# Kernel optimization log

Measured on AMD Instinct MI355X. Metric: run time of the kernel, lower is better.

## Reference

```python
import jax, jax.numpy as jnp
import numpy as np

N_NODES = 50000
N_EDGES = 800000
N_GRAPHS = 1024
H = 128          # hidden_dim
L = 5            # n_conv_layers
NODE_IN = 4
EDGE_IN = 41
N_TARGETS = 3
EPS = 1e-5


def _ln(x, g, b):
    m = jnp.mean(x, axis=-1, keepdims=True)
    v = jnp.var(x, axis=-1, keepdims=True)
    return (x - m) / jnp.sqrt(v + EPS) * g + b


def setup_inputs() -> dict:
    key = jax.random.key(0)
    ks = jax.random.split(key, 24)
    w = lambda k, shp: (jax.random.normal(k, shp, dtype=jnp.float32) * 0.05)
    inp = {
        "atom_fea": jax.random.normal(ks[0], (N_NODES, NODE_IN), dtype=jnp.float32),
        "nbr_fea": jax.random.normal(ks[1], (N_EDGES, EDGE_IN), dtype=jnp.float32),
        "nbr_idx": jax.random.randint(ks[2], (N_EDGES, 2), 0, N_NODES, dtype=jnp.int32),
        "batch_mapping": jnp.sort(jax.random.randint(ks[3], (N_NODES,), 0, N_GRAPHS, dtype=jnp.int32)),
        # node embedding: Linear(4->H) + LayerNorm + SiLU
        "emb_w": w(ks[4], (NODE_IN, H)), "emb_b": jnp.zeros((H,), jnp.float32),
        "emb_ln_g": jnp.ones((H,), jnp.float32), "emb_ln_b": jnp.zeros((H,), jnp.float32),
        # edge embedding: Linear(41->H) + SiLU
        "edge_w": w(ks[5], (EDGE_IN, H)), "edge_b": jnp.zeros((H,), jnp.float32),
        # conv layers: Linear(2H->2H), SiLU, Linear(2H->H), SiLU; stacked over L
        "conv_w1": w(ks[6], (L, 2 * H, 2 * H)), "conv_b1": jnp.zeros((L, 2 * H), jnp.float32),
        "conv_w2": w(ks[7], (L, 2 * H, H)), "conv_b2": jnp.zeros((L, H), jnp.float32),
        "ln_g": jnp.ones((L, H), jnp.float32), "ln_b": jnp.zeros((L, H), jnp.float32),
        # output head
        "out_w1": w(ks[8], (H, H)), "out_b1": jnp.zeros((H,), jnp.float32),
        "out_w2": w(ks[9], (H, H // 2)), "out_b2": jnp.zeros((H // 2,), jnp.float32),
        "out_w3": w(ks[10], (H // 2, N_TARGETS)), "out_b3": jnp.zeros((N_TARGETS,), jnp.float32),
    }
    return inp


def reference(atom_fea, nbr_fea, nbr_idx, batch_mapping,
              emb_w, emb_b, emb_ln_g, emb_ln_b, edge_w, edge_b,
              conv_w1, conv_b1, conv_w2, conv_b2, ln_g, ln_b,
              out_w1, out_b1, out_w2, out_b2, out_w3, out_b3):
    silu = jax.nn.silu
    # embeddings (dropout is eval-mode identity)
    x = silu(_ln(atom_fea @ emb_w + emb_b, emb_ln_g, emb_ln_b))      # [N, H]
    e = silu(nbr_fea @ edge_w + edge_b)                               # [E, H]
    src, dst = nbr_idx[:, 0], nbr_idx[:, 1]
    n = x.shape[0]
    # per-node incoming edge counts (same every layer)
    cnt = jax.ops.segment_sum(jnp.ones_like(dst, dtype=x.dtype), dst, num_segments=n)
    cnt = jnp.clip(cnt, 1.0)[:, None]
    for i in range(L):
        m = jnp.concatenate([x[src], e], axis=1)                      # [E, 2H] gather
        m = silu(m @ conv_w1[i] + conv_b1[i])                         # [E, 2H]
        m = silu(m @ conv_w2[i] + conv_b2[i])                         # [E, H]
        aggr = jax.ops.segment_sum(m, dst, num_segments=n) / cnt      # scatter-mean
        x = _ln(x + aggr, ln_g[i], ln_b[i])                           # residual + LN
    # graph-level mean pooling
    gcnt = jax.ops.segment_sum(jnp.ones((n,), x.dtype), batch_mapping, num_segments=N_GRAPHS)
    gcnt = jnp.clip(gcnt, 1.0)[:, None]
    crystal = jax.ops.segment_sum(x, batch_mapping, num_segments=N_GRAPHS) / gcnt  # [G, H]
    h = silu(crystal @ out_w1 + out_b1)
    h = silu(h @ out_w2 + out_b2)
    return h @ out_w3 + out_b3                                        # [G, n_targets]
```

## Files before the change

kernel.cpp:

```cpp
#include <hip/hip_runtime.h>
#include <hip/hip_bf16.h>
#include <math.h>

#define N_NODES 50000
#define N_EDGES 800000
#define N_GRAPHS 1024
#define HD 128
#define NLAYERS 5
#define EDGE_IN 41
#define NT 3
#define LN_EPS 1e-5f

typedef unsigned int uint;
typedef unsigned short ushort;
typedef __attribute__((ext_vector_type(8))) short short8;
typedef __attribute__((ext_vector_type(4))) float f32x4;

__device__ __forceinline__ float silu_f(float v) {
    return v * __builtin_amdgcn_rcpf(1.0f + __expf(-v));
}

__device__ __forceinline__ ushort f2bf(float f) {
    uint u = __float_as_uint(f);
    u = u + 0x7FFFu + ((u >> 16) & 1u);
    return (ushort)(u >> 16);
}

__device__ __forceinline__ short8 ld16(const ushort* p) {
    union { int4 i; short8 s; } u;
    u.i = *(const int4*)p;
    return u.s;
}

__device__ __forceinline__ f32x4 mfma16(short8 a, short8 b, f32x4 c) {
    return __builtin_amdgcn_mfma_f32_16x16x32_bf16(a, b, c, 0, 0, 0);
}

__device__ __forceinline__ void wave_lds_fence() {
    __asm__ volatile("s_waitcnt lgkmcnt(0)" ::: "memory");
}

__device__ __forceinline__ void cp16(const ushort* g, ushort* l) {
    __builtin_amdgcn_global_load_lds(
        (const __attribute__((address_space(1))) unsigned int*)g,
        (__attribute__((address_space(3))) unsigned int*)l, 16, 0, 0);
}

__device__ __forceinline__ void stage4k(ushort* lds, const ushort* g, int w, int L) {
#pragma unroll
    for (int i = 0; i < 2; ++i) {
        int f = w * 1024 + i * 512;
        cp16(g + f + L * 8, lds + f);
    }
}

__global__ void k_zero(float* __restrict__ p, int n) {
    int i = blockIdx.x * 256 + threadIdx.x;
    if (i < n) p[i] = 0.0f;
}

__global__ void k_hist(const int* __restrict__ nbr_idx, int* __restrict__ cnt_i) {
    int i = blockIdx.x * 256 + threadIdx.x;
    if (i < N_EDGES) atomicAdd(&cnt_i[nbr_idx[2 * i + 1]], 1);
}

__global__ __launch_bounds__(256) void k_scan(
    const int* __restrict__ cnt_i, int* __restrict__ cur, float* __restrict__ cntf)
{
    __shared__ int warpsum[4];
    __shared__ int srun;
    int tid = threadIdx.x;
    int lane = tid & 63, wv = tid >> 6;
    if (tid == 0) srun = 0;
    __syncthreads();
    for (int base = 0; base < N_NODES; base += 256) {
        int i = base + tid;
        int c = (i < N_NODES) ? cnt_i[i] : 0;
        int s = c;
        for (int off = 1; off < 64; off <<= 1) {
            int t = __shfl_up(s, off);
            if (lane >= off) s += t;
        }
        if (lane == 63) warpsum[wv] = s;
        __syncthreads();
        int woff = 0;
        for (int k = 0; k < wv; ++k) woff += warpsum[k];
        int run = srun;
        if (i < N_NODES) {
            cur[i]  = run + woff + s - c;
            cntf[i] = (float)c;
        }
        __syncthreads();
        if (tid == 255) srun = run + woff + s;
    }
}

__global__ void k_scatter(const int* __restrict__ nbr_idx, int* __restrict__ cur,
                          int* __restrict__ ssrc, int* __restrict__ sdst,
                          int* __restrict__ posof)
{
    int e = blockIdx.x * 256 + threadIdx.x;
    if (e < N_EDGES) {
        int s = nbr_idx[2 * e];
        int d = nbr_idx[2 * e + 1];
        int p = atomicAdd(&cur[d], 1);
        ssrc[p] = s;
        sdst[p] = d;
        posof[e] = p;
    }
}

__global__ void k_swz_w1(const float* __restrict__ w1, ushort* __restrict__ w1s) {
    int i = blockIdx.x * 256 + threadIdx.x;
    int l = i >> 16;
    int r = i & 65535;
    int j = r & 7, L = (r >> 3) & 63, s = (r >> 9) & 7, c = (r >> 12) & 15;
    int k = 32 * s + ((L >> 4) & 3) * 8 + j;
    int n = 16 * c + (L & 15);
    w1s[i] = f2bf(w1[(size_t)l * 65536 + k * 256 + n]);
}
__global__ void k_swz_w2(const float* __restrict__ w2, ushort* __restrict__ w2s) {
    int i = blockIdx.x * 256 + threadIdx.x;
    int l = i >> 15;
    int r = i & 32767;
    int j = r & 7, L = (r >> 3) & 63, t = (r >> 9) & 7, s2 = (r >> 12) & 7;
    int k = 32 * s2 + ((L >> 4) & 3) * 8 + j;
    int n = 16 * t + (L & 15);
    w2s[i] = f2bf(w2[(size_t)l * 32768 + k * 128 + n]);
}

__global__ __launch_bounds__(128) void k_node_embed(
    const float* __restrict__ atom, const float* __restrict__ w,
    const float* __restrict__ b, const float* __restrict__ g,
    const float* __restrict__ bet, float* __restrict__ x, ushort* __restrict__ x_bf)
{
    int node = blockIdx.x;
    int h = threadIdx.x;
    float4 a = *(const float4*)(atom + (size_t)node * 4);
    float acc = b[h] + a.x * w[h] + a.y * w[HD + h] + a.z * w[2 * HD + h] + a.w * w[3 * HD + h];
    __shared__ float s1[2], s2[2];
    float sum = acc, sq = acc * acc;
    for (int off = 32; off > 0; off >>= 1) { sum += __shfl_down(sum, off); sq += __shfl_down(sq, off); }
    int wid = h >> 6, lane = h & 63;
    if (lane == 0) { s1[wid] = sum; s2[wid] = sq; }
    __syncthreads();
    float m = (s1[0] + s1[1]) * (1.0f / 128.0f);
    float v = (s2[0] + s2[1]) * (1.0f / 128.0f) - m * m;
    float y = (acc - m) * rsqrtf(v + LN_EPS) * g[h] + bet[h];
    y = silu_f(y);
    x[(size_t)node * HD + h] = y;
    x_bf[(size_t)node * HD + h] = f2bf(y);
}

#define ETILE 32
__global__ __launch_bounds__(128) void k_edge_embed(
    const float* __restrict__ fea, const float* __restrict__ w,
    const float* __restrict__ b, const int* __restrict__ posof,
    ushort* __restrict__ e_bf)
{
    __shared__ float sf[ETILE][EDGE_IN + 1];
    int e0 = blockIdx.x * ETILE;
    int tid = threadIdx.x;
    for (int i = tid; i < ETILE * EDGE_IN; i += 128) {
        int m = i / EDGE_IN, k = i % EDGE_IN;
        sf[m][k] = fea[(size_t)(e0 + m) * EDGE_IN + k];
    }
    __syncthreads();
    float bb = b[tid];
    float acc[ETILE];
#pragma unroll
    for (int m = 0; m < ETILE; m++) acc[m] = bb;
    for (int k = 0; k < EDGE_IN; k++) {
        float wk = w[k * HD + tid];
#pragma unroll
        for (int m = 0; m < ETILE; m++) acc[m] += sf[m][k] * wk;
    }
#pragma unroll
    for (int m = 0; m < ETILE; m++) {
        int p = posof[e0 + m];
        e_bf[(size_t)p * HD + tid] = f2bf(silu_f(acc[m]));
    }
}

__global__ void k_gcount(const int* __restrict__ bm, float* __restrict__ gcnt) {
    int i = blockIdx.x * 256 + threadIdx.x;
    if (i < N_NODES) atomicAdd(&gcnt[bm[i]], 1.0f);
}

#define M1CP 40
#define RSTR 18
__global__ __launch_bounds__(256, 3) void k_conv_mfma(
    const ushort* __restrict__ x_bf, const ushort* __restrict__ e_bf,
    const int* __restrict__ ssrc, const int* __restrict__ sdst,
    const ushort* __restrict__ w1s, const float* __restrict__ cb1,
    const ushort* __restrict__ w2s, const float* __restrict__ cb2,
    float* __restrict__ aggr)
{
    __shared__ __align__(16) ushort sW1[2][4096];
    __shared__ __align__(16) ushort sW2[4096];
    __shared__ __align__(16) ushort sM1[4][32 * M1CP];
    __shared__ int sDst[128];

    int tid = threadIdx.x;
    int w = tid >> 6;
    int L = tid & 63;
    int m = L & 15;
    int quad = L >> 4;
    int eb = blockIdx.x * 128;
    int ew = eb + w * 32;

    if (tid < 128) sDst[tid] = sdst[eb + tid];

    short8 af[2][8];
#pragma unroll
    for (int t = 0; t < 2; ++t) {
        int src = ssrc[ew + t * 16 + m];
        const ushort* xr = x_bf + (size_t)src * HD + quad * 8;
        const ushort* er = e_bf + (size_t)(ew + t * 16 + m) * HD + quad * 8;
#pragma unroll
        for (int s = 0; s < 4; ++s) af[t][s] = ld16(xr + 32 * s);
#pragma unroll
        for (int s = 0; s < 4; ++s) af[t][4 + s] = ld16(er + 32 * s);
    }

    f32x4 acc2[2][8];
#pragma unroll
    for (int t = 0; t < 2; ++t)
#pragma unroll
        for (int tt = 0; tt < 8; ++tt)
#pragma unroll
            for (int r = 0; r < 4; ++r) acc2[t][tt][r] = 0.0f;

    ushort* sm = sM1[w];

    stage4k(sW1[0], w1s, w, L);
    stage4k(sW2, w2s, w, L);

    for (int p = 0; p < 16; ++p) {
        __syncthreads();
        if (p < 15) stage4k(sW1[(p + 1) & 1], w1s + (p + 1) * 4096, w, L);
        if (!(p & 1) && p >= 2)
            stage4k(sW2, w2s + (p >> 1) * 4096, w, L);

        f32x4 p0, p1;
#pragma unroll
        for (int r = 0; r < 4; ++r) { p0[r] = 0.0f; p1[r] = 0.0f; }
        const ushort* wb = sW1[p & 1] + L * 8;
#pragma unroll
        for (int s = 0; s < 8; ++s) {
            short8 wv = ld16(wb + s * 512);
            p0 = mfma16(af[0][s], wv, p0);
            p1 = mfma16(af[1][s], wv, p1);
        }

        float bv = cb1[p * 16 + m];
        int hb = (p & 1) * 16;
#pragma unroll
        for (int r = 0; r < 4; ++r) {
            sm[(quad * 4 + r) * M1CP + hb + m]        = f2bf(silu_f(p0[r] + bv));
            sm[(16 + quad * 4 + r) * M1CP + hb + m]   = f2bf(silu_f(p1[r] + bv));
        }

        if (p & 1) {
            wave_lds_fence();
            short8 a20 = ld16(sm + m * M1CP + quad * 8);
            short8 a21 = ld16(sm + (16 + m) * M1CP + quad * 8);
            const ushort* w2p = sW2 + L * 8;
#pragma unroll
            for (int tt = 0; tt < 8; ++tt) {
                short8 bf = ld16(w2p + tt * 512);
                acc2[0][tt] = mfma16(a20, bf, acc2[0][tt]);
                acc2[1][tt] = mfma16(a21, bf, acc2[1][tt]);
            }
            wave_lds_fence();
        }
    }

    float* sRed = (float*)sW1;
    int tcol = tid & 15;
    int row0 = (tid >> 4) * 8;
#pragma unroll
    for (int tt = 0; tt < 8; ++tt) {
        __syncthreads();
        float bv = cb2[tt * 16 + m];
#pragma unroll
        for (int t = 0; t < 2; ++t)
#pragma unroll
            for (int r = 0; r < 4; ++r)
                sRed[(w * 32 + t * 16 + quad * 4 + r) * RSTR + m] =
                    silu_f(acc2[t][tt][r] + bv);
        __syncthreads();
        float s = sRed[row0 * RSTR + tcol];
        int cd = sDst[row0];
        for (int i = 1; i < 8; ++i) {
            int rr = row0 + i;
            int d2 = sDst[rr];
            float v = sRed[rr * RSTR + tcol];
            if (d2 == cd) {
                s += v;
            } else {
                atomicAdd(aggr + (size_t)cd * HD + tt * 16 + tcol, s);
                cd = d2;
                s = v;
            }
        }
        atomicAdd(aggr + (size_t)cd * HD + tt * 16 + tcol, s);
    }
}

__global__ __launch_bounds__(128) void k_post(
    float* __restrict__ aggr, const float* __restrict__ cnt,
    const float* __restrict__ g, const float* __restrict__ bet,
    float* __restrict__ x, ushort* __restrict__ x_bf)
{
    int node = blockIdx.x;
    int h = threadIdx.x;
    float inv = __builtin_amdgcn_rcpf(fmaxf(cnt[node], 1.0f));
    float av = aggr[(size_t)node * HD + h];
    aggr[(size_t)node * HD + h] = 0.0f;
    float acc = x[(size_t)node * HD + h] + av * inv;
    __shared__ float s1[2], s2[2];
    float sum = acc, sq = acc * acc;
    for (int off = 32; off > 0; off >>= 1) { sum += __shfl_down(sum, off); sq += __shfl_down(sq, off); }
    int wid = h >> 6, lane = h & 63;
    if (lane == 0) { s1[wid] = sum; s2[wid] = sq; }
    __syncthreads();
    float m = (s1[0] + s1[1]) * (1.0f / 128.0f);
    float v = (s2[0] + s2[1]) * (1.0f / 128.0f) - m * m;
    float y = (acc - m) * rsqrtf(v + LN_EPS) * g[h] + bet[h];
    x[(size_t)node * HD + h] = y;
    x_bf[(size_t)node * HD + h] = f2bf(y);
}

__global__ __launch_bounds__(128) void k_gaggr(
    const float* __restrict__ x, const int* __restrict__ bm,
    float* __restrict__ crystal)
{
    int node = blockIdx.x;
    int h = threadIdx.x;
    atomicAdd(&crystal[(size_t)bm[node] * HD + h], x[(size_t)node * HD + h]);
}

__global__ __launch_bounds__(128) void k_readout(
    const float* __restrict__ crystal, const float* __restrict__ gcnt,
    const float* __restrict__ w1, const float* __restrict__ b1,
    const float* __restrict__ w2, const float* __restrict__ b2,
    const float* __restrict__ w3, const float* __restrict__ b3,
    float* __restrict__ out)
{
    int gph = blockIdx.x;
    int t = threadIdx.x;
    __shared__ float sc[HD], sh1[HD], sh2[64];
    float inv = __builtin_amdgcn_rcpf(fmaxf(gcnt[gph], 1.0f));
    sc[t] = crystal[(size_t)gph * HD + t] * inv;
    __syncthreads();
    float acc = b1[t];
    for (int k = 0; k < HD; k++) acc += sc[k] * w1[k * HD + t];
    sh1[t] = silu_f(acc);
    __syncthreads();
    if (t < 64) {
        float a2 = b2[t];
        for (int k = 0; k < HD; k++) a2 += sh1[k] * w2[k * 64 + t];
        sh2[t] = silu_f(a2);
    }
    __syncthreads();
    if (t < NT) {
        float a3 = b3[t];
        for (int k = 0; k < 64; k++) a3 += sh2[k] * w3[k * NT + t];
        out[(size_t)gph * NT + t] = a3;
    }
}

extern "C" void kernel_launch(void* const* d_in, const int* in_sizes, int n_in,
                              void* d_out, int out_size, void* d_ws, size_t ws_size,
                              hipStream_t stream)
{
    const float* atom_fea = (const float*)d_in[0];
    const float* nbr_fea  = (const float*)d_in[1];
    const int*   nbr_idx  = (const int*)d_in[2];
    const int*   bm       = (const int*)d_in[3];
    const float* emb_w    = (const float*)d_in[4];
    const float* emb_b    = (const float*)d_in[5];
    const float* emb_ln_g = (const float*)d_in[6];
    const float* emb_ln_b = (const float*)d_in[7];
    const float* edge_w   = (const float*)d_in[8];
    const float* edge_b   = (const float*)d_in[9];
    const float* conv_w1  = (const float*)d_in[10];
    const float* conv_b1  = (const float*)d_in[11];
    const float* conv_w2  = (const float*)d_in[12];
    const float* conv_b2  = (const float*)d_in[13];
    const float* ln_g     = (const float*)d_in[14];
    const float* ln_b     = (const float*)d_in[15];
    const float* out_w1   = (const float*)d_in[16];
    const float* out_b1   = (const float*)d_in[17];
    const float* out_w2   = (const float*)d_in[18];
    const float* out_b2   = (const float*)d_in[19];
    const float* out_w3   = (const float*)d_in[20];
    const float* out_b3   = (const float*)d_in[21];
    float* out = (float*)d_out;

    char* base = (char*)d_ws;
    size_t off = 0;
    auto alloc = [&](size_t bytes) -> char* {
        char* p = base + off;
        off = (off + bytes + 255) & ~(size_t)255;
        return p;
    };
    float*  xbuf    = (float*) alloc((size_t)N_NODES * HD * 4);
    float*  aggr    = (float*) alloc((size_t)N_NODES * HD * 4);
    float*  cnt     = (float*) alloc((size_t)N_NODES * 4);
    float*  crystal = (float*) alloc((size_t)N_GRAPHS * HD * 4);
    float*  gcnt    = (float*) alloc((size_t)N_GRAPHS * 4);
    ushort* x_bf    = (ushort*)alloc((size_t)N_NODES * HD * 2);
    ushort* e_bf    = (ushort*)alloc((size_t)N_EDGES * HD * 2);
    ushort* w1s     = (ushort*)alloc((size_t)NLAYERS * 65536 * 2);
    ushort* w2s     = (ushort*)alloc((size_t)NLAYERS * 32768 * 2);
    int*    cnt_i   = (int*)   alloc((size_t)N_NODES * 4);
    int*    cur     = (int*)   alloc((size_t)N_NODES * 4);
    int*    ssrc    = (int*)   alloc((size_t)N_EDGES * 4);
    int*    sdst    = (int*)   alloc((size_t)N_EDGES * 4);
    int*    posof   = (int*)   alloc((size_t)N_EDGES * 4);

    k_swz_w1<<<(NLAYERS * 65536) / 256, 256, 0, stream>>>(conv_w1, w1s);
    k_swz_w2<<<(NLAYERS * 32768) / 256, 256, 0, stream>>>(conv_w2, w2s);

    k_zero<<<(N_NODES * HD) / 256, 256, 0, stream>>>(aggr, N_NODES * HD);
    int zn = N_NODES + N_GRAPHS * HD + N_GRAPHS + 128;
    k_zero<<<(zn + 255) / 256, 256, 0, stream>>>(cnt, zn);
    k_zero<<<(N_NODES + 255) / 256, 256, 0, stream>>>((float*)cnt_i, N_NODES);

    k_hist<<<N_EDGES / 256, 256, 0, stream>>>(nbr_idx, cnt_i);
    k_scan<<<1, 256, 0, stream>>>(cnt_i, cur, cnt);
    k_scatter<<<N_EDGES / 256, 256, 0, stream>>>(nbr_idx, cur, ssrc, sdst, posof);

    k_node_embed<<<N_NODES, 128, 0, stream>>>(atom_fea, emb_w, emb_b, emb_ln_g, emb_ln_b, xbuf, x_bf);
    k_edge_embed<<<N_EDGES / ETILE, 128, 0, stream>>>(nbr_fea, edge_w, edge_b, posof, e_bf);
    k_gcount<<<(N_NODES + 255) / 256, 256, 0, stream>>>(bm, gcnt);

    for (int l = 0; l < NLAYERS; ++l) {
        k_conv_mfma<<<N_EDGES / 128, 256, 0, stream>>>(
            x_bf, e_bf, ssrc, sdst,
            w1s + (size_t)l * 65536, conv_b1 + (size_t)l * 256,
            w2s + (size_t)l * 32768, conv_b2 + (size_t)l * 128,
            aggr);
        k_post<<<N_NODES, 128, 0, stream>>>(aggr, cnt, ln_g + (size_t)l * HD, ln_b + (size_t)l * HD, xbuf, x_bf);
    }

    k_gaggr<<<N_NODES, 128, 0, stream>>>(xbuf, bm, crystal);
    k_readout<<<N_GRAPHS, 128, 0, stream>>>(crystal, gcnt, out_w1, out_b1, out_w2, out_b2, out_w3, out_b3, out);
}
```

Before: 2.333 ms.

## Split MFMA accumulator chains, raise wave priority, drop LDS waits, vectorize post-LN

```diff
diff --git a/kernel.cpp b/kernel.cpp
--- a/kernel.cpp
+++ b/kernel.cpp
@@ -15,6 +15,7 @@
 typedef unsigned short ushort;
 typedef __attribute__((ext_vector_type(8))) short short8;
 typedef __attribute__((ext_vector_type(4))) float f32x4;
+typedef __attribute__((ext_vector_type(4))) ushort us4;
 
 __device__ __forceinline__ float silu_f(float v) {
     return v * __builtin_amdgcn_rcpf(1.0f + __expf(-v));
@@ -36,8 +37,8 @@
     return __builtin_amdgcn_mfma_f32_16x16x32_bf16(a, b, c, 0, 0, 0);
 }
 
-__device__ __forceinline__ void wave_lds_fence() {
-    __asm__ volatile("s_waitcnt lgkmcnt(0)" ::: "memory");
+__device__ __forceinline__ void compiler_fence() {
+    __asm__ volatile("" ::: "memory");
 }
 
 __device__ __forceinline__ void cp16(const ushort* g, ushort* l) {
@@ -64,16 +65,16 @@
     if (i < N_EDGES) atomicAdd(&cnt_i[nbr_idx[2 * i + 1]], 1);
 }
 
-__global__ __launch_bounds__(256) void k_scan(
+__global__ __launch_bounds__(1024) void k_scan(
     const int* __restrict__ cnt_i, int* __restrict__ cur, float* __restrict__ cntf)
 {
-    __shared__ int warpsum[4];
+    __shared__ int warpsum[16];
     __shared__ int srun;
     int tid = threadIdx.x;
     int lane = tid & 63, wv = tid >> 6;
     if (tid == 0) srun = 0;
     __syncthreads();
-    for (int base = 0; base < N_NODES; base += 256) {
+    for (int base = 0; base < N_NODES; base += 1024) {
         int i = base + tid;
         int c = (i < N_NODES) ? cnt_i[i] : 0;
         int s = c;
@@ -91,7 +92,7 @@
             cntf[i] = (float)c;
         }
         __syncthreads();
-        if (tid == 255) srun = run + woff + s;
+        if (tid == 1023) srun = run + woff + s;
     }
 }
 
@@ -242,16 +243,26 @@
         if (!(p & 1) && p >= 2)
             stage4k(sW2, w2s + (p >> 1) * 4096, w, L);
 
-        f32x4 p0, p1;
-#pragma unroll
-        for (int r = 0; r < 4; ++r) { p0[r] = 0.0f; p1[r] = 0.0f; }
+        f32x4 p0a, p0b, p1a, p1b;
+#pragma unroll
+        for (int r = 0; r < 4; ++r) { p0a[r] = 0.0f; p0b[r] = 0.0f; p1a[r] = 0.0f; p1b[r] = 0.0f; }
         const ushort* wb = sW1[p & 1] + L * 8;
-#pragma unroll
-        for (int s = 0; s < 8; ++s) {
+        __builtin_amdgcn_s_setprio(1);
+#pragma unroll
+        for (int s = 0; s < 4; ++s) {
             short8 wv = ld16(wb + s * 512);
-            p0 = mfma16(af[0][s], wv, p0);
-            p1 = mfma16(af[1][s], wv, p1);
-        }
+            p0a = mfma16(af[0][s], wv, p0a);
+            p1a = mfma16(af[1][s], wv, p1a);
+        }
+#pragma unroll
+        for (int s = 4; s < 8; ++s) {
+            short8 wv = ld16(wb + s * 512);
+            p0b = mfma16(af[0][s], wv, p0b);
+            p1b = mfma16(af[1][s], wv, p1b);
+        }
+        __builtin_amdgcn_s_setprio(0);
+        f32x4 p0 = p0a + p0b;
+        f32x4 p1 = p1a + p1b;
 
         float bv = cb1[p * 16 + m];
         int hb = (p & 1) * 16;
@@ -262,17 +273,19 @@
         }
 
         if (p & 1) {
-            wave_lds_fence();
+            compiler_fence();
             short8 a20 = ld16(sm + m * M1CP + quad * 8);
             short8 a21 = ld16(sm + (16 + m) * M1CP + quad * 8);
             const ushort* w2p = sW2 + L * 8;
+            __builtin_amdgcn_s_setprio(1);
 #pragma unroll
             for (int tt = 0; tt < 8; ++tt) {
                 short8 bf = ld16(w2p + tt * 512);
                 acc2[0][tt] = mfma16(a20, bf, acc2[0][tt]);
                 acc2[1][tt] = mfma16(a21, bf, acc2[1][tt]);
             }
-            wave_lds_fence();
+            __builtin_amdgcn_s_setprio(0);
+            compiler_fence();
         }
     }
 
@@ -308,28 +321,45 @@
     }
 }
 
-__global__ __launch_bounds__(128) void k_post(
+__global__ __launch_bounds__(256) void k_post(
     float* __restrict__ aggr, const float* __restrict__ cnt,
     const float* __restrict__ g, const float* __restrict__ bet,
     float* __restrict__ x, ushort* __restrict__ x_bf)
 {
-    int node = blockIdx.x;
-    int h = threadIdx.x;
+    int t = threadIdx.x;
+    int node = blockIdx.x * 8 + (t >> 5);
+    int c = (t & 31) * 4;
+    size_t base = (size_t)node * HD + c;
     float inv = __builtin_amdgcn_rcpf(fmaxf(cnt[node], 1.0f));
-    float av = aggr[(size_t)node * HD + h];
-    aggr[(size_t)node * HD + h] = 0.0f;
-    float acc = x[(size_t)node * HD + h] + av * inv;
-    __shared__ float s1[2], s2[2];
-    float sum = acc, sq = acc * acc;
-    for (int off = 32; off > 0; off >>= 1) { sum += __shfl_down(sum, off); sq += __shfl_down(sq, off); }
-    int wid = h >> 6, lane = h & 63;
-    if (lane == 0) { s1[wid] = sum; s2[wid] = sq; }
-    __syncthreads();
-    float m = (s1[0] + s1[1]) * (1.0f / 128.0f);
-    float v = (s2[0] + s2[1]) * (1.0f / 128.0f) - m * m;
-    float y = (acc - m) * rsqrtf(v + LN_EPS) * g[h] + bet[h];
-    x[(size_t)node * HD + h] = y;
-    x_bf[(size_t)node * HD + h] = f2bf(y);
+    f32x4 av = *(f32x4*)(aggr + base);
+    f32x4 z; z[0] = 0.0f; z[1] = 0.0f; z[2] = 0.0f; z[3] = 0.0f;
+    *(f32x4*)(aggr + base) = z;
+    f32x4 xv = *(const f32x4*)(x + base);
+    f32x4 acc;
+#pragma unroll
+    for (int j = 0; j < 4; ++j) acc[j] = xv[j] + av[j] * inv;
+    float sum = acc[0] + acc[1] + acc[2] + acc[3];
+    float sq  = acc[0]*acc[0] + acc[1]*acc[1] + acc[2]*acc[2] + acc[3]*acc[3];
+    for (int off = 16; off > 0; off >>= 1) {
+        sum += __shfl_down(sum, off, 32);
+        sq  += __shfl_down(sq,  off, 32);
+    }
+    float msum = __shfl(sum, 0, 32);
+    float msq  = __shfl(sq,  0, 32);
+    float mean = msum * (1.0f / 128.0f);
+    float var  = msq * (1.0f / 128.0f) - mean * mean;
+    float rstd = rsqrtf(var + LN_EPS);
+    f32x4 gv = *(const f32x4*)(g + c);
+    f32x4 bv = *(const f32x4*)(bet + c);
+    f32x4 y;
+    us4 ybf;
+#pragma unroll
+    for (int j = 0; j < 4; ++j) {
+        y[j] = (acc[j] - mean) * rstd * gv[j] + bv[j];
+        ybf[j] = f2bf(y[j]);
+    }
+    *(f32x4*)(x + base) = y;
+    *(us4*)(x_bf + base) = ybf;
 }
 
 __global__ __launch_bounds__(128) void k_gaggr(
@@ -430,7 +460,7 @@
     k_zero<<<(N_NODES + 255) / 256, 256, 0, stream>>>((float*)cnt_i, N_NODES);
 
     k_hist<<<N_EDGES / 256, 256, 0, stream>>>(nbr_idx, cnt_i);
-    k_scan<<<1, 256, 0, stream>>>(cnt_i, cur, cnt);
+    k_scan<<<1, 1024, 0, stream>>>(cnt_i, cur, cnt);
     k_scatter<<<N_EDGES / 256, 256, 0, stream>>>(nbr_idx, cur, ssrc, sdst, posof);
 
     k_node_embed<<<N_NODES, 128, 0, stream>>>(atom_fea, emb_w, emb_b, emb_ln_g, emb_ln_b, xbuf, x_bf);
@@ -443,7 +473,7 @@
             w1s + (size_t)l * 65536, conv_b1 + (size_t)l * 256,
             w2s + (size_t)l * 32768, conv_b2 + (size_t)l * 128,
             aggr);
-        k_post<<<N_NODES, 128, 0, stream>>>(aggr, cnt, ln_g + (size_t)l * HD, ln_b + (size_t)l * HD, xbuf, x_bf);
+        k_post<<<N_NODES / 8, 256, 0, stream>>>(aggr, cnt, ln_g + (size_t)l * HD, ln_b + (size_t)l * HD, xbuf, x_bf);
     }
 
     k_gaggr<<<N_NODES, 128, 0, stream>>>(xbuf, bm, crystal);
```

New measurement: 2.251 ms. 1.04x faster.
